# Kernel tuning notes

Measured on AMD Instinct MI355X. Metric: run time of the kernel, lower is better.

The kernel has to match this reference:

```python
import jax, jax.numpy as jnp
import numpy as np

T, N, E, IN_DIM, H = 20, 50000, 800000, 16, 128
NPF = 7  # num_physical_features
EPS = 1e-5


def setup_inputs() -> dict:
    key = jax.random.key(0)
    ks = jax.random.split(key, 24)
    s = 0.05
    inp = {
        'x': jax.random.normal(ks[0], (T, N, IN_DIM), jnp.float32),
        'edge_index': jax.random.randint(ks[1], (2, E), 0, N, jnp.int64),
        # SAGEConv layer 1 (PyG: lin_l on aggregated neighbors w/ bias, lin_r on root no bias)
        'sage1_wl': jax.random.normal(ks[2], (IN_DIM, H), jnp.float32) * s,
        'sage1_bl': jnp.zeros((H,), jnp.float32),
        'sage1_wr': jax.random.normal(ks[3], (IN_DIM, H), jnp.float32) * s,
        # SAGEConv layer 2
        'sage2_wl': jax.random.normal(ks[4], (H, H), jnp.float32) * s,
        'sage2_bl': jnp.zeros((H,), jnp.float32),
        'sage2_wr': jax.random.normal(ks[5], (H, H), jnp.float32) * s,
        # LayerNorm
        'ln_g': jnp.ones((H,), jnp.float32),
        'ln_b': jnp.zeros((H,), jnp.float32),
        # GRU (torch layout: [3H, H], gate order r,z,n)
        'gru_wih': jax.random.normal(ks[6], (3 * H, H), jnp.float32) * s,
        'gru_whh': jax.random.normal(ks[7], (3 * H, H), jnp.float32) * s,
        'gru_bih': jnp.zeros((3 * H,), jnp.float32),
        'gru_bhh': jnp.zeros((3 * H,), jnp.float32),
        # Thickness decoder
        'th_w1': jax.random.normal(ks[8], (H, H), jnp.float32) * s,
        'th_b1': jnp.zeros((H,), jnp.float32),
        'th_w2': jax.random.normal(ks[9], (H, 1), jnp.float32) * s,
        'th_b2': jnp.zeros((1,), jnp.float32),
        # Physical feature decoder
        'ph_w1': jax.random.normal(ks[10], (H, H), jnp.float32) * s,
        'ph_b1': jnp.zeros((H,), jnp.float32),
        'ph_w2': jax.random.normal(ks[11], (H, NPF), jnp.float32) * s,
        'ph_b2': jnp.zeros((NPF,), jnp.float32),
    }
    return inp


def _sage(h, src, dst, deg_inv, wl, bl, wr):
    # mean-aggregate neighbor features over incoming edges, then two linears
    agg = jax.ops.segment_sum(h[src], dst, num_segments=N) * deg_inv[:, None]
    return agg @ wl + bl + h @ wr


def _forward(x, edge_index,
             sage1_wl, sage1_bl, sage1_wr,
             sage2_wl, sage2_bl, sage2_wr,
             ln_g, ln_b,
             gru_wih, gru_whh, gru_bih, gru_bhh,
             th_w1, th_b1, th_w2, th_b2,
             ph_w1, ph_b1, ph_w2, ph_b2):
    src, dst = edge_index[0], edge_index[1]
    deg = jax.ops.segment_sum(jnp.ones((E,), jnp.float32), dst, num_segments=N)
    deg_inv = 1.0 / jnp.maximum(deg, 1.0)

    def encode(xt):  # [N, IN_DIM] -> [N, H]
        h = jax.nn.relu(_sage(xt, src, dst, deg_inv, sage1_wl, sage1_bl, sage1_wr))
        h = jax.nn.relu(_sage(h, src, dst, deg_inv, sage2_wl, sage2_bl, sage2_wr))
        mu = jnp.mean(h, axis=-1, keepdims=True)
        var = jnp.mean(jnp.square(h - mu), axis=-1, keepdims=True)
        return (h - mu) * jax.lax.rsqrt(var + EPS) * ln_g + ln_b

    encoded = jax.lax.map(encode, x)  # [T, N, H]

    # GRU over time, batch = nodes
    def gru_step(h, x_t):
        gi = x_t @ gru_wih.T + gru_bih  # [N, 3H]
        gh = h @ gru_whh.T + gru_bhh
        i_r, i_z, i_n = jnp.split(gi, 3, axis=-1)
        h_r, h_z, h_n = jnp.split(gh, 3, axis=-1)
        r = jax.nn.sigmoid(i_r + h_r)
        z = jax.nn.sigmoid(i_z + h_z)
        n = jnp.tanh(i_n + r * h_n)
        h_new = (1.0 - z) * n + z * h
        return h_new, h_new

    h0 = jnp.zeros((N, H), jnp.float32)
    _, h_temporal = jax.lax.scan(gru_step, h0, encoded)  # [T, N, H]

    th = jax.nn.relu(h_temporal @ th_w1 + th_b1) @ th_w2 + th_b2   # [T, N, 1]
    ph = jax.nn.relu(h_temporal @ ph_w1 + ph_b1) @ ph_w2 + ph_b2   # [T, N, NPF]
    return th, ph


def reference(x, edge_index,
              sage1_wl, sage1_bl, sage1_wr,
              sage2_wl, sage2_bl, sage2_wr,
              ln_g, ln_b,
              gru_wih, gru_whh, gru_bih, gru_bhh,
              th_w1, th_b1, th_w2, th_b2,
              ph_w1, ph_b1, ph_w2, ph_b2):
    return _forward(x, edge_index,
                    sage1_wl, sage1_bl, sage1_wr,
                    sage2_wl, sage2_bl, sage2_wr,
                    ln_g, ln_b,
                    gru_wih, gru_whh, gru_bih, gru_bhh,
                    th_w1, th_b1, th_w2, th_b2,
                    ph_w1, ph_b1, ph_w2, ph_b2)
```

## Files before the change

kernel.cpp:

```cpp
#include <hip/hip_runtime.h>
#include <hip/hip_bf16.h>

#define TT 20
#define NN 50000
#define EE 800000
#define IND 16
#define HH 128
#define NPF 7
#define CC 4
#define NB ((NN + 255) / 256)

typedef __attribute__((ext_vector_type(8))) short bf16x8;
typedef __attribute__((ext_vector_type(4))) float f32x4;
#define MFMA(a, b, c) __builtin_amdgcn_mfma_f32_16x16x32_bf16(a, b, c, 0, 0, 0)

__device__ __forceinline__ unsigned short f2bf(float f) {
    union { float f; unsigned u; } v; v.f = f;
    unsigned r = v.u + 0x7fffu + ((v.u >> 16) & 1u);
    return (unsigned short)(r >> 16);
}
__device__ __forceinline__ float bf2f(unsigned short u) {
    union { unsigned u; float f; } v; v.u = ((unsigned)u) << 16;
    return v.f;
}

__global__ void detect_kernel(const int* ei, int* flag, int E) {
    __shared__ int nz;
    if (threadIdx.x == 0) nz = 0;
    __syncthreads();
    for (int i = threadIdx.x; i < 1024 && i < E; i += blockDim.x)
        if (ei[2 * i + 1] != 0) atomicOr(&nz, 1);
    __syncthreads();
    if (threadIdx.x == 0) *flag = (nz == 0) ? 1 : 0;
}
__device__ __forceinline__ int edge_src(const int* ei, int e, int E, int f) {
    return f ? ei[2 * e] : ei[e];
}
__device__ __forceinline__ int edge_dst(const int* ei, int e, int E, int f) {
    return f ? ei[2 * (E + e)] : ei[E + e];
}
__global__ void count_deg_kernel(const int* ei, const int* flag, int* deg, int E) {
    int e = blockIdx.x * blockDim.x + threadIdx.x;
    if (e >= E) return;
    int f = *flag;
    atomicAdd(&deg[edge_dst(ei, e, E, f)], 1);
}

__global__ __launch_bounds__(256) void sum_blocks_kernel(const int* deg, int* bsum) {
    int i = blockIdx.x * 256 + threadIdx.x;
    int v = (i < NN) ? deg[i] : 0;
#pragma unroll
    for (int o = 1; o <= 32; o <<= 1) v += __shfl_xor(v, o);
    __shared__ int ws[4];
    if ((threadIdx.x & 63) == 0) ws[threadIdx.x >> 6] = v;
    __syncthreads();
    if (threadIdx.x == 0) bsum[blockIdx.x] = ws[0] + ws[1] + ws[2] + ws[3];
}
__global__ __launch_bounds__(256) void scan_blocks_kernel(const int* bsum, int* bbase) {
    __shared__ int arr[256];
    int t = threadIdx.x;
    int v = (t < NB) ? bsum[t] : 0;
    arr[t] = v;
    __syncthreads();
    for (int off = 1; off < 256; off <<= 1) {
        int u = (t >= off) ? arr[t - off] : 0;
        __syncthreads();
        arr[t] += u;
        __syncthreads();
    }
    if (t < NB) bbase[t] = arr[t] - v;
}
__global__ __launch_bounds__(256) void offs_kernel(const int* deg, const int* bbase,
                                                   int* offs, int* cursor,
                                                   float* dinv, int E) {
    __shared__ int arr[256];
    int t = threadIdx.x;
    int i = blockIdx.x * 256 + t;
    int d = (i < NN) ? deg[i] : 0;
    arr[t] = d;
    __syncthreads();
    for (int off = 1; off < 256; off <<= 1) {
        int u = (t >= off) ? arr[t - off] : 0;
        __syncthreads();
        arr[t] += u;
        __syncthreads();
    }
    if (i < NN) {
        int o = bbase[blockIdx.x] + arr[t] - d;
        offs[i] = o;
        cursor[i] = o;
        dinv[i] = 1.0f / (float)(d > 1 ? d : 1);
        if (i == NN - 1) offs[NN] = E;
    }
}
__global__ void fill_csr_kernel(const int* ei, const int* flag, int* cursor,
                                int* csr, int E) {
    int e = blockIdx.x * blockDim.x + threadIdx.x;
    if (e >= E) return;
    int f = *flag;
    int s = edge_src(ei, e, E, f);
    int d = edge_dst(ei, e, E, f);
    int p = atomicAdd(&cursor[d], 1);
    csr[p] = s;
}

__global__ void pack_kernel(const float* src, unsigned short* dst, int tiles,
                            int mode) {
    int id = blockIdx.x * blockDim.x + threadIdx.x;
    if (id >= tiles * 4 * 64) return;
    int lane = id & 63, kk = (id >> 6) & 3, tile = id >> 8;
    int n = tile * 16 + (lane & 15);
    int kbase = kk * 32 + (lane >> 4) * 8;
    unsigned short out[8];
#pragma unroll
    for (int i = 0; i < 8; ++i) {
        int k = kbase + i;
        float v = mode ? src[n * HH + k] : src[k * (tiles * 16) + n];
        out[i] = f2bf(v);
    }
    *(uint4*)(dst + (size_t)id * 8) = *(uint4*)out;
}

__global__ __launch_bounds__(128) void sage1_kernel(
    const float* __restrict__ x, const int* __restrict__ offs,
    const int* __restrict__ csr, const float* __restrict__ dinv,
    const float* __restrict__ wl, const float* __restrict__ bl,
    const float* __restrict__ wr, unsigned short* __restrict__ h1c, int t0) {
    const int tid = threadIdx.x;
    const int ci = blockIdx.y;
    const float* xt = x + (size_t)(t0 + ci) * NN * IND;
    const int m0 = blockIdx.x * 8;
    __shared__ __align__(16) float sAgg[8][IND];
    __shared__ float sX[8][IND];
    {
        int r = tid >> 4, node = m0 + r;
        int l16 = tid & 15, sub = l16 >> 2, q = l16 & 3;
        int e1 = offs[node + 1];
        float4 a0 = make_float4(0.f, 0.f, 0.f, 0.f);
        float4 a1 = make_float4(0.f, 0.f, 0.f, 0.f);
        float4 a2 = make_float4(0.f, 0.f, 0.f, 0.f);
        float4 a3 = make_float4(0.f, 0.f, 0.f, 0.f);
        int e = offs[node] + sub;
        for (; e + 12 < e1; e += 16) {
            int s0 = __builtin_nontemporal_load(&csr[e]);
            int s1 = __builtin_nontemporal_load(&csr[e + 4]);
            int s2 = __builtin_nontemporal_load(&csr[e + 8]);
            int s3 = __builtin_nontemporal_load(&csr[e + 12]);
            float4 v0 = *(const float4*)(xt + (size_t)s0 * IND + q * 4);
            float4 v1 = *(const float4*)(xt + (size_t)s1 * IND + q * 4);
            float4 v2 = *(const float4*)(xt + (size_t)s2 * IND + q * 4);
            float4 v3 = *(const float4*)(xt + (size_t)s3 * IND + q * 4);
            a0.x += v0.x; a0.y += v0.y; a0.z += v0.z; a0.w += v0.w;
            a1.x += v1.x; a1.y += v1.y; a1.z += v1.z; a1.w += v1.w;
            a2.x += v2.x; a2.y += v2.y; a2.z += v2.z; a2.w += v2.w;
            a3.x += v3.x; a3.y += v3.y; a3.z += v3.z; a3.w += v3.w;
        }
        for (; e < e1; e += 4) {
            int s0 = __builtin_nontemporal_load(&csr[e]);
            float4 v0 = *(const float4*)(xt + (size_t)s0 * IND + q * 4);
            a0.x += v0.x; a0.y += v0.y; a0.z += v0.z; a0.w += v0.w;
        }
        float4 acc;
        acc.x = a0.x + a1.x + a2.x + a3.x;
        acc.y = a0.y + a1.y + a2.y + a3.y;
        acc.z = a0.z + a1.z + a2.z + a3.z;
        acc.w = a0.w + a1.w + a2.w + a3.w;
#pragma unroll
        for (int o = 4; o <= 8; o <<= 1) {
            acc.x += __shfl_xor(acc.x, o);
            acc.y += __shfl_xor(acc.y, o);
            acc.z += __shfl_xor(acc.z, o);
            acc.w += __shfl_xor(acc.w, o);
        }
        if (sub == 0) {
            float di = dinv[node];
            acc.x *= di; acc.y *= di; acc.z *= di; acc.w *= di;
            *(float4*)&sAgg[r][q * 4] = acc;
        }
        sX[r][l16] = xt[(size_t)node * IND + l16];
    }
    __syncthreads();
    const int col = tid;
    float acc[8];
    float b = bl[col];
#pragma unroll
    for (int m = 0; m < 8; ++m) acc[m] = b;
#pragma unroll
    for (int k = 0; k < IND; ++k) {
        float wlv = wl[k * HH + col];
        float wrv = wr[k * HH + col];
#pragma unroll
        for (int m = 0; m < 8; ++m) acc[m] += sAgg[m][k] * wlv + sX[m][k] * wrv;
    }
#pragma unroll
    for (int m = 0; m < 8; ++m)
        h1c[((size_t)(m0 + m) * CC + ci) * HH + col] = f2bf(fmaxf(acc[m], 0.f));
}

#define ADD8(acc, v) do {                                     \
    union { unsigned u; float f; } t_;                        \
    t_.u = (v).x << 16;         acc[0] += t_.f;               \
    t_.u = (v).x & 0xffff0000u; acc[1] += t_.f;               \
    t_.u = (v).y << 16;         acc[2] += t_.f;               \
    t_.u = (v).y & 0xffff0000u; acc[3] += t_.f;               \
    t_.u = (v).z << 16;         acc[4] += t_.f;               \
    t_.u = (v).z & 0xffff0000u; acc[5] += t_.f;               \
    t_.u = (v).w << 16;         acc[6] += t_.f;               \
    t_.u = (v).w & 0xffff0000u; acc[7] += t_.f;               \
} while (0)

__global__ __launch_bounds__(256) void sage2_agg_kernel(
    const unsigned short* __restrict__ h1c, const int* __restrict__ offs,
    const int* __restrict__ csr, const float* __restrict__ dinv,
    unsigned short* __restrict__ agg2c) {
    const int wid = threadIdx.x >> 6, lane = threadIdx.x & 63;
    const int n = blockIdx.x * 4 + wid;
    const char* __restrict__ tb = (const char*)h1c;
    const int lb = lane * 16;
    const int e0 = offs[n], e1 = offs[n + 1];
    float A[8][8];
#pragma unroll
    for (int u = 0; u < 8; ++u)
#pragma unroll
        for (int j = 0; j < 8; ++j) A[u][j] = 0.f;
    int e = e0;
    for (; e + 7 < e1; e += 8) {
        int s[8];
#pragma unroll
        for (int u = 0; u < 8; ++u) s[u] = csr[e + u];
        uint4 v[8];
#pragma unroll
        for (int u = 0; u < 8; ++u)
            v[u] = *(const uint4*)(tb + (size_t)s[u] * 1024 + lb);
#pragma unroll
        for (int u = 0; u < 8; ++u) ADD8(A[u], v[u]);
    }
    for (; e < e1; ++e) {
        int s0 = csr[e];
        uint4 v0 = *(const uint4*)(tb + (size_t)s0 * 1024 + lb);
        ADD8(A[0], v0);
    }
    float di = dinv[n];
    unsigned short o[8];
#pragma unroll
    for (int j = 0; j < 8; ++j) {
        float s = ((A[0][j] + A[1][j]) + (A[2][j] + A[3][j])) +
                  ((A[4][j] + A[5][j]) + (A[6][j] + A[7][j]));
        o[j] = f2bf(s * di);
    }
    *(uint4*)((char*)agg2c + (size_t)n * 1024 + lb) = *(uint4*)o;
}

#define LDA(buf, kk)                                                          \
    (*(const bf16x8*)((const char*)(buf) +                                    \
        (((lane & 15) * 256 + (kk) * 64 + (lane >> 4) * 16) ^                 \
         (((lane & 15) & 7) << 4))))

__global__ __launch_bounds__(64) void gru_fused_kernel(
    const unsigned short* __restrict__ agg2c, const unsigned short* __restrict__ h1c,
    const unsigned short* __restrict__ pS2L, const unsigned short* __restrict__ pS2R,
    const float* __restrict__ s2bl, const float* __restrict__ lng,
    const float* __restrict__ lnb,
    const unsigned short* __restrict__ pGI, const unsigned short* __restrict__ pGH,
    const float* __restrict__ bih, const float* __restrict__ bhh,
    float* __restrict__ h, unsigned short* __restrict__ hallc, int ci) {
    const int lane = threadIdx.x;
    const int r0 = blockIdx.x * 16;
    __shared__ unsigned short bufA[16 * 128];
    __shared__ unsigned short bufB[16 * 128];
    __shared__ unsigned short bufH[16 * 128];

#pragma unroll
    for (int j = 0; j < 4; ++j) {
        int off = (lane + 64 * j) * 16;
        int row = off >> 8, colb = off & 255;
        int swz = off ^ ((row & 7) << 4);
        size_t src = (size_t)(r0 + row) * 1024 + (size_t)ci * 256 + colb;
        *(uint4*)((char*)bufA + swz) = *(const uint4*)((const char*)agg2c + src);
        *(uint4*)((char*)bufB + swz) = *(const uint4*)((const char*)h1c + src);
        const float* hs = h + (size_t)r0 * HH + (size_t)(off / 2);
        unsigned short tmp[8];
#pragma unroll
        for (int i = 0; i < 8; ++i) tmp[i] = f2bf(hs[i]);
        *(uint4*)((char*)bufH + swz) = *(uint4*)tmp;
    }
    __syncthreads();

    bf16x8 ae[4], ah[4];
#pragma unroll
    for (int kk = 0; kk < 4; ++kk) { ae[kk] = LDA(bufA, kk); ah[kk] = LDA(bufB, kk); }
    float vE[8][4];
    float sS[4] = {0, 0, 0, 0}, sQ[4] = {0, 0, 0, 0};
#pragma unroll
    for (int c = 0; c < 8; ++c) {
        f32x4 al = {0, 0, 0, 0}, ar = {0, 0, 0, 0};
#pragma unroll
        for (int kk = 0; kk < 4; ++kk) {
            bf16x8 bl = *(const bf16x8*)(pS2L + ((size_t)(c * 4 + kk) * 64 + lane) * 8);
            bf16x8 br = *(const bf16x8*)(pS2R + ((size_t)(c * 4 + kk) * 64 + lane) * 8);
            al = MFMA(ae[kk], bl, al);
            ar = MFMA(ah[kk], br, ar);
        }
        int col = c * 16 + (lane & 15);
        float bb = s2bl[col];
#pragma unroll
        for (int j = 0; j < 4; ++j) {
            float v = fmaxf(al[j] + ar[j] + bb, 0.f);
            vE[c][j] = v; sS[j] += v; sQ[j] += v * v;
        }
    }
#pragma unroll
    for (int o = 1; o <= 8; o <<= 1) {
#pragma unroll
        for (int j = 0; j < 4; ++j) {
            sS[j] += __shfl_xor(sS[j], o);
            sQ[j] += __shfl_xor(sQ[j], o);
        }
    }
    __syncthreads();
#pragma unroll
    for (int c = 0; c < 8; ++c) {
        int col = c * 16 + (lane & 15);
        float g = lng[col], b = lnb[col];
#pragma unroll
        for (int j = 0; j < 4; ++j) {
            float mu = sS[j] * (1.f / 128.f);
            float var = sQ[j] * (1.f / 128.f) - mu * mu;
            float ve = (vE[c][j] - mu) * rsqrtf(var + 1e-5f) * g + b;
            int row = (lane >> 4) * 4 + j;
            int off = ((row * 128 + col) * 2) ^ ((row & 7) << 4);
            *(unsigned short*)((char*)bufA + off) = f2bf(ve);
        }
    }
    __syncthreads();

    bf16x8 xe[4], xh[4];
#pragma unroll
    for (int kk = 0; kk < 4; ++kk) { xe[kk] = LDA(bufA, kk); xh[kk] = LDA(bufH, kk); }
#pragma unroll
    for (int c = 0; c < 8; ++c) {
        f32x4 air = {0,0,0,0}, aiz = {0,0,0,0}, ain = {0,0,0,0};
        f32x4 ahr = {0,0,0,0}, ahz = {0,0,0,0}, ahn = {0,0,0,0};
#pragma unroll
        for (int kk = 0; kk < 4; ++kk) {
            bf16x8 bir = *(const bf16x8*)(pGI + ((size_t)((c     ) * 4 + kk) * 64 + lane) * 8);
            bf16x8 biz = *(const bf16x8*)(pGI + ((size_t)((c +  8) * 4 + kk) * 64 + lane) * 8);
            bf16x8 bin = *(const bf16x8*)(pGI + ((size_t)((c + 16) * 4 + kk) * 64 + lane) * 8);
            bf16x8 bhr = *(const bf16x8*)(pGH + ((size_t)((c     ) * 4 + kk) * 64 + lane) * 8);
            bf16x8 bhz = *(const bf16x8*)(pGH + ((size_t)((c +  8) * 4 + kk) * 64 + lane) * 8);
            bf16x8 bhn = *(const bf16x8*)(pGH + ((size_t)((c + 16) * 4 + kk) * 64 + lane) * 8);
            air = MFMA(xe[kk], bir, air); aiz = MFMA(xe[kk], biz, aiz);
            ain = MFMA(xe[kk], bin, ain);
            ahr = MFMA(xh[kk], bhr, ahr); ahz = MFMA(xh[kk], bhz, ahz);
            ahn = MFMA(xh[kk], bhn, ahn);
        }
        int col = c * 16 + (lane & 15);
        float bir_ = bih[col], biz_ = bih[HH + col], bin_ = bih[2 * HH + col];
        float bhr_ = bhh[col], bhz_ = bhh[HH + col], bhn_ = bhh[2 * HH + col];
#pragma unroll
        for (int j = 0; j < 4; ++j) {
            int row = (lane >> 4) * 4 + j;
            size_t gidx = (size_t)(r0 + row) * HH + col;
            float rr = 1.f / (1.f + expf(-(air[j] + bir_ + ahr[j] + bhr_)));
            float zz = 1.f / (1.f + expf(-(aiz[j] + biz_ + ahz[j] + bhz_)));
            float nn2 = tanhf(ain[j] + bin_ + rr * (ahn[j] + bhn_));
            float hold = h[gidx];
            float hnew = (1.f - zz) * nn2 + zz * hold;
            h[gidx] = hnew;
            hallc[((size_t)(r0 + row) * CC + ci) * HH + col] = f2bf(hnew);
        }
    }
}

__global__ __launch_bounds__(64) void dec_kernel(
    const unsigned short* __restrict__ hall,
    const unsigned short* __restrict__ pT1, const unsigned short* __restrict__ pP1,
    const float* __restrict__ tb1, const float* __restrict__ tw2,
    const float* __restrict__ tb2, const float* __restrict__ pb1,
    const float* __restrict__ pw2, const float* __restrict__ pb2,
    float* __restrict__ out_th, float* __restrict__ out_ph, int t0) {
    const int lane = threadIdx.x;
    const int rc = blockIdx.x * 16;
    const int ci = rc / NN;
    const int n0 = rc - ci * NN;
    const int tg = t0 + ci;
    __shared__ unsigned short bufB[16 * 128];
#pragma unroll
    for (int j = 0; j < 4; ++j) {
        int off = (lane + 64 * j) * 16;
        int row = off >> 8, colb = off & 255;
        int swz = off ^ ((row & 7) << 4);
        *(uint4*)((char*)bufB + swz) =
            *(const uint4*)((const char*)hall +
                            (size_t)(n0 + row) * 1024 + (size_t)ci * 256 + colb);
    }
    __syncthreads();
    bf16x8 xd[4];
#pragma unroll
    for (int kk = 0; kk < 4; ++kk) xd[kk] = LDA(bufB, kk);
    float pt[4] = {0, 0, 0, 0};
    float pf[NPF][4];
#pragma unroll
    for (int f = 0; f < NPF; ++f)
#pragma unroll
        for (int j = 0; j < 4; ++j) pf[f][j] = 0.f;
#pragma unroll
    for (int c = 0; c < 8; ++c) {
        f32x4 at = {0, 0, 0, 0}, ap = {0, 0, 0, 0};
#pragma unroll
        for (int kk = 0; kk < 4; ++kk) {
            bf16x8 bt = *(const bf16x8*)(pT1 + ((size_t)(c * 4 + kk) * 64 + lane) * 8);
            bf16x8 bp = *(const bf16x8*)(pP1 + ((size_t)(c * 4 + kk) * 64 + lane) * 8);
            at = MFMA(xd[kk], bt, at);
            ap = MFMA(xd[kk], bp, ap);
        }
        int col = c * 16 + (lane & 15);
        float b1 = tb1[col], b2 = pb1[col], w2 = tw2[col];
        float wp[NPF];
#pragma unroll
        for (int f = 0; f < NPF; ++f) wp[f] = pw2[col * NPF + f];
#pragma unroll
        for (int j = 0; j < 4; ++j) {
            float a = fmaxf(at[j] + b1, 0.f);
            pt[j] += a * w2;
            float p = fmaxf(ap[j] + b2, 0.f);
#pragma unroll
            for (int f = 0; f < NPF; ++f) pf[f][j] += p * wp[f];
        }
    }
#pragma unroll
    for (int o = 1; o <= 8; o <<= 1) {
#pragma unroll
        for (int j = 0; j < 4; ++j) {
            pt[j] += __shfl_xor(pt[j], o);
#pragma unroll
            for (int f = 0; f < NPF; ++f) pf[f][j] += __shfl_xor(pf[f][j], o);
        }
    }
    if ((lane & 15) == 0) {
        int g = lane >> 4;
#pragma unroll
        for (int j = 0; j < 4; ++j) {
            int gr = n0 + g * 4 + j;
            out_th[(size_t)tg * NN + gr] = pt[j] + tb2[0];
#pragma unroll
            for (int f = 0; f < NPF; ++f)
                out_ph[((size_t)tg * NN + gr) * NPF + f] = pf[f][j] + pb2[f];
        }
    }
}
#undef LDA

extern "C" void kernel_launch(void* const* d_in, const int* in_sizes, int n_in,
                              void* d_out, int out_size, void* d_ws, size_t ws_size,
                              hipStream_t stream) {
    const float* x     = (const float*)d_in[0];
    const int*   ei    = (const int*)d_in[1];
    const float* s1wl  = (const float*)d_in[2];
    const float* s1bl  = (const float*)d_in[3];
    const float* s1wr  = (const float*)d_in[4];
    const float* s2wl  = (const float*)d_in[5];
    const float* s2bl  = (const float*)d_in[6];
    const float* s2wr  = (const float*)d_in[7];
    const float* lng   = (const float*)d_in[8];
    const float* lnb   = (const float*)d_in[9];
    const float* g_wih = (const float*)d_in[10];
    const float* g_whh = (const float*)d_in[11];
    const float* g_bih = (const float*)d_in[12];
    const float* g_bhh = (const float*)d_in[13];
    const float* tw1   = (const float*)d_in[14];
    const float* tb1   = (const float*)d_in[15];
    const float* tw2   = (const float*)d_in[16];
    const float* tb2   = (const float*)d_in[17];
    const float* pw1   = (const float*)d_in[18];
    const float* pb1   = (const float*)d_in[19];
    const float* pw2   = (const float*)d_in[20];
    const float* pb2   = (const float*)d_in[21];

    char* ws = (char*)d_ws;
    size_t o = 0;
    auto alloc = [&](size_t bytes) {
        size_t r = o;
        o += (bytes + 255) & ~(size_t)255;
        return r;
    };
    int*            flag  = (int*)(ws + alloc(4));
    int*            deg   = (int*)(ws + alloc((size_t)NN * 4));
    int*            offs  = (int*)(ws + alloc((size_t)(NN + 1) * 4));
    int*            curs  = (int*)(ws + alloc((size_t)NN * 4));
    int*            csr   = (int*)(ws + alloc((size_t)EE * 4));
    float*          dinv  = (float*)(ws + alloc((size_t)NN * 4));
    int*            bsum  = (int*)(ws + alloc((size_t)NB * 4));
    int*            bbase = (int*)(ws + alloc((size_t)NB * 4));
    unsigned short* pS2L  = (unsigned short*)(ws + alloc(8 * 4 * 64 * 8 * 2));
    unsigned short* pS2R  = (unsigned short*)(ws + alloc(8 * 4 * 64 * 8 * 2));
    unsigned short* pT1   = (unsigned short*)(ws + alloc(8 * 4 * 64 * 8 * 2));
    unsigned short* pP1   = (unsigned short*)(ws + alloc(8 * 4 * 64 * 8 * 2));
    unsigned short* pGI   = (unsigned short*)(ws + alloc(24 * 4 * 64 * 8 * 2));
    unsigned short* pGH   = (unsigned short*)(ws + alloc(24 * 4 * 64 * 8 * 2));
    float*          hbuf  = (float*)(ws + alloc((size_t)NN * HH * 4));
    unsigned short* h1c   = (unsigned short*)(ws + alloc((size_t)NN * CC * HH * 2));
    unsigned short* agg2c = (unsigned short*)(ws + alloc((size_t)NN * CC * HH * 2));
    unsigned short* hallc = agg2c;

    detect_kernel<<<1, 256, 0, stream>>>(ei, flag, EE);
    hipMemsetAsync(deg, 0, (size_t)NN * 4, stream);
    count_deg_kernel<<<(EE + 255) / 256, 256, 0, stream>>>(ei, flag, deg, EE);
    sum_blocks_kernel<<<NB, 256, 0, stream>>>(deg, bsum);
    scan_blocks_kernel<<<1, 256, 0, stream>>>(bsum, bbase);
    offs_kernel<<<NB, 256, 0, stream>>>(deg, bbase, offs, curs, dinv, EE);
    fill_csr_kernel<<<(EE + 255) / 256, 256, 0, stream>>>(ei, flag, curs, csr, EE);
    pack_kernel<<<(8 * 4 * 64 + 255) / 256, 256, 0, stream>>>(s2wl, pS2L, 8, 0);
    pack_kernel<<<(8 * 4 * 64 + 255) / 256, 256, 0, stream>>>(s2wr, pS2R, 8, 0);
    pack_kernel<<<(8 * 4 * 64 + 255) / 256, 256, 0, stream>>>(tw1, pT1, 8, 0);
    pack_kernel<<<(8 * 4 * 64 + 255) / 256, 256, 0, stream>>>(pw1, pP1, 8, 0);
    pack_kernel<<<(24 * 4 * 64 + 255) / 256, 256, 0, stream>>>(g_wih, pGI, 24, 1);
    pack_kernel<<<(24 * 4 * 64 + 255) / 256, 256, 0, stream>>>(g_whh, pGH, 24, 1);
    hipMemsetAsync(hbuf, 0, (size_t)NN * HH * 4, stream);

    float* out = (float*)d_out;
    for (int t0 = 0; t0 < TT; t0 += CC) {
        dim3 g1(NN / 8, CC);
        sage1_kernel<<<g1, 128, 0, stream>>>(x, offs, csr, dinv, s1wl, s1bl,
                                             s1wr, h1c, t0);
        sage2_agg_kernel<<<NN / 4, 256, 0, stream>>>(h1c, offs, csr, dinv, agg2c);
        for (int ci = 0; ci < CC; ++ci) {
            gru_fused_kernel<<<NN / 16, 64, 0, stream>>>(
                agg2c, h1c, pS2L, pS2R, s2bl, lng, lnb, pGI, pGH,
                g_bih, g_bhh, hbuf, hallc, ci);
        }
        dec_kernel<<<CC * NN / 16, 64, 0, stream>>>(
            hallc, pT1, pP1, tb1, tw2, tb2, pb1, pw2, pb2,
            out, out + (size_t)TT * NN, t0);
    }
}
```

Before: 2.636 ms.

## Split encoder from GRU and keep hidden state in LDS across chunk timesteps

The fused per-timestep GRU kernel is split in two. An encoder kernel (SAGE2 linears plus LayerNorm) now runs over all chunk timesteps in one launch and writes its result in place into the aggregation buffer. A GRU loop kernel then keeps the fp32 hidden state of its 16 rows in swizzled LDS across the 4 timesteps, so it no longer reloads and stores h in global memory every step and needs fewer launches. The weight-pack launches are also merged into one kernel, and the sage2 aggregation drops from 8-way to 4-way unrolled accumulation, which lowers register pressure but exposes less memory-level parallelism. The encoded activations now make an extra round trip through global memory.

Measured after the change: 5.195 ms. +97.1%, slower.

```diff
diff --git a/kernel.cpp b/kernel.cpp
--- a/kernel.cpp
+++ b/kernel.cpp
@@ -104,21 +104,32 @@
     csr[p] = s;
 }
 
-__global__ void pack_kernel(const float* src, unsigned short* dst, int tiles,
-                            int mode) {
+__global__ void pack_all_kernel(
+    const float* s2wl, const float* s2wr, const float* tw1, const float* pw1,
+    const float* wih, const float* whh,
+    unsigned short* pS2L, unsigned short* pS2R, unsigned short* pT1,
+    unsigned short* pP1, unsigned short* pGI, unsigned short* pGH) {
     int id = blockIdx.x * blockDim.x + threadIdx.x;
-    if (id >= tiles * 4 * 64) return;
-    int lane = id & 63, kk = (id >> 6) & 3, tile = id >> 8;
+    if (id >= 80 * 256) return;
+    int gt = id >> 8;
+    int lane = id & 63, kk = (id >> 6) & 3;
+    const float* src; unsigned short* dst; int tile, mode, ncols;
+    if (gt < 8)       { src = s2wl; dst = pS2L; tile = gt;      mode = 0; ncols = 128; }
+    else if (gt < 16) { src = s2wr; dst = pS2R; tile = gt - 8;  mode = 0; ncols = 128; }
+    else if (gt < 24) { src = tw1;  dst = pT1;  tile = gt - 16; mode = 0; ncols = 128; }
+    else if (gt < 32) { src = pw1;  dst = pP1;  tile = gt - 24; mode = 0; ncols = 128; }
+    else if (gt < 56) { src = wih;  dst = pGI;  tile = gt - 32; mode = 1; ncols = 384; }
+    else              { src = whh;  dst = pGH;  tile = gt - 56; mode = 1; ncols = 384; }
     int n = tile * 16 + (lane & 15);
     int kbase = kk * 32 + (lane >> 4) * 8;
     unsigned short out[8];
 #pragma unroll
     for (int i = 0; i < 8; ++i) {
         int k = kbase + i;
-        float v = mode ? src[n * HH + k] : src[k * (tiles * 16) + n];
+        float v = mode ? src[n * HH + k] : src[k * ncols + n];
         out[i] = f2bf(v);
     }
-    *(uint4*)(dst + (size_t)id * 8) = *(uint4*)out;
+    *(uint4*)(dst + ((size_t)tile * 256 + kk * 64 + lane) * 8) = *(uint4*)out;
 }
 
 __global__ __launch_bounds__(128) void sage1_kernel(
@@ -218,36 +229,26 @@
     const char* __restrict__ tb = (const char*)h1c;
     const int lb = lane * 16;
     const int e0 = offs[n], e1 = offs[n + 1];
-    float A[8][8];
-#pragma unroll
-    for (int u = 0; u < 8; ++u)
-#pragma unroll
-        for (int j = 0; j < 8; ++j) A[u][j] = 0.f;
+    float a[8] = {0,0,0,0,0,0,0,0}, b[8] = {0,0,0,0,0,0,0,0};
+    float c_[8] = {0,0,0,0,0,0,0,0}, d[8] = {0,0,0,0,0,0,0,0};
     int e = e0;
-    for (; e + 7 < e1; e += 8) {
-        int s[8];
-#pragma unroll
-        for (int u = 0; u < 8; ++u) s[u] = csr[e + u];
-        uint4 v[8];
-#pragma unroll
-        for (int u = 0; u < 8; ++u)
-            v[u] = *(const uint4*)(tb + (size_t)s[u] * 1024 + lb);
-#pragma unroll
-        for (int u = 0; u < 8; ++u) ADD8(A[u], v[u]);
+    for (; e + 3 < e1; e += 4) {
+        int s0 = csr[e], s1 = csr[e + 1], s2 = csr[e + 2], s3 = csr[e + 3];
+        uint4 v0 = *(const uint4*)(tb + (size_t)s0 * 1024 + lb);
+        uint4 v1 = *(const uint4*)(tb + (size_t)s1 * 1024 + lb);
+        uint4 v2 = *(const uint4*)(tb + (size_t)s2 * 1024 + lb);
+        uint4 v3 = *(const uint4*)(tb + (size_t)s3 * 1024 + lb);
+        ADD8(a, v0); ADD8(b, v1); ADD8(c_, v2); ADD8(d, v3);
     }
     for (; e < e1; ++e) {
         int s0 = csr[e];
         uint4 v0 = *(const uint4*)(tb + (size_t)s0 * 1024 + lb);
-        ADD8(A[0], v0);
+        ADD8(a, v0);
     }
     float di = dinv[n];
     unsigned short o[8];
 #pragma unroll
-    for (int j = 0; j < 8; ++j) {
-        float s = ((A[0][j] + A[1][j]) + (A[2][j] + A[3][j])) +
-                  ((A[4][j] + A[5][j]) + (A[6][j] + A[7][j]));
-        o[j] = f2bf(s * di);
-    }
+    for (int j = 0; j < 8; ++j) o[j] = f2bf((a[j] + b[j] + c_[j] + d[j]) * di);
     *(uint4*)((char*)agg2c + (size_t)n * 1024 + lb) = *(uint4*)o;
 }
 
@@ -256,20 +257,16 @@
         (((lane & 15) * 256 + (kk) * 64 + (lane >> 4) * 16) ^                 \
          (((lane & 15) & 7) << 4))))
 
-__global__ __launch_bounds__(64) void gru_fused_kernel(
-    const unsigned short* __restrict__ agg2c, const unsigned short* __restrict__ h1c,
+__global__ __launch_bounds__(64) void enc_kernel(
+    unsigned short* __restrict__ agg2c, const unsigned short* __restrict__ h1c,
     const unsigned short* __restrict__ pS2L, const unsigned short* __restrict__ pS2R,
     const float* __restrict__ s2bl, const float* __restrict__ lng,
-    const float* __restrict__ lnb,
-    const unsigned short* __restrict__ pGI, const unsigned short* __restrict__ pGH,
-    const float* __restrict__ bih, const float* __restrict__ bhh,
-    float* __restrict__ h, unsigned short* __restrict__ hallc, int ci) {
+    const float* __restrict__ lnb) {
     const int lane = threadIdx.x;
     const int r0 = blockIdx.x * 16;
+    const int ci = blockIdx.y;
     __shared__ unsigned short bufA[16 * 128];
     __shared__ unsigned short bufB[16 * 128];
-    __shared__ unsigned short bufH[16 * 128];
-
 #pragma unroll
     for (int j = 0; j < 4; ++j) {
         int off = (lane + 64 * j) * 16;
@@ -278,14 +275,8 @@
         size_t src = (size_t)(r0 + row) * 1024 + (size_t)ci * 256 + colb;
         *(uint4*)((char*)bufA + swz) = *(const uint4*)((const char*)agg2c + src);
         *(uint4*)((char*)bufB + swz) = *(const uint4*)((const char*)h1c + src);
-        const float* hs = h + (size_t)r0 * HH + (size_t)(off / 2);
-        unsigned short tmp[8];
-#pragma unroll
-        for (int i = 0; i < 8; ++i) tmp[i] = f2bf(hs[i]);
-        *(uint4*)((char*)bufH + swz) = *(uint4*)tmp;
-    }
-    __syncthreads();
-
+    }
+    __syncthreads();
     bf16x8 ae[4], ah[4];
 #pragma unroll
     for (int kk = 0; kk < 4; ++kk) { ae[kk] = LDA(bufA, kk); ah[kk] = LDA(bufB, kk); }
@@ -333,42 +324,107 @@
         }
     }
     __syncthreads();
-
-    bf16x8 xe[4], xh[4];
-#pragma unroll
-    for (int kk = 0; kk < 4; ++kk) { xe[kk] = LDA(bufA, kk); xh[kk] = LDA(bufH, kk); }
-#pragma unroll
-    for (int c = 0; c < 8; ++c) {
-        f32x4 air = {0,0,0,0}, aiz = {0,0,0,0}, ain = {0,0,0,0};
-        f32x4 ahr = {0,0,0,0}, ahz = {0,0,0,0}, ahn = {0,0,0,0};
+#pragma unroll
+    for (int j = 0; j < 4; ++j) {
+        int off = (lane + 64 * j) * 16;
+        int row = off >> 8, colb = off & 255;
+        int swz = off ^ ((row & 7) << 4);
+        size_t src = (size_t)(r0 + row) * 1024 + (size_t)ci * 256 + colb;
+        *(uint4*)((char*)agg2c + src) = *(const uint4*)((const char*)bufA + swz);
+    }
+}
+
+__global__ __launch_bounds__(64) void gru_loop_kernel(
+    const unsigned short* __restrict__ encc,
+    const unsigned short* __restrict__ pGI, const unsigned short* __restrict__ pGH,
+    const float* __restrict__ bih, const float* __restrict__ bhh,
+    float* __restrict__ h, unsigned short* __restrict__ hallc) {
+    const int lane = threadIdx.x;
+    const int r0 = blockIdx.x * 16;
+    const int fr = lane & 15;
+    const int rg = (lane >> 4) * 4;
+    __shared__ unsigned short bufA[16 * 128];
+    __shared__ float          bufHF[16 * 128];
+
+#pragma unroll
+    for (int j = 0; j < 8; ++j) {
+        int off = (lane + 64 * j) * 16;
+        int row = off >> 9;
+        int swz = off ^ ((row & 7) << 5);
+        *(uint4*)((char*)bufHF + swz) =
+            *(const uint4*)((const char*)(h + (size_t)r0 * HH) + off);
+    }
+    __syncthreads();
+
+#pragma unroll 1
+    for (int ci = 0; ci < CC; ++ci) {
+#pragma unroll
+        for (int j = 0; j < 4; ++j) {
+            int off = (lane + 64 * j) * 16;
+            int row = off >> 8, colb = off & 255;
+            int swz = off ^ ((row & 7) << 4);
+            size_t src = (size_t)(r0 + row) * 1024 + (size_t)ci * 256 + colb;
+            *(uint4*)((char*)bufA + swz) = *(const uint4*)((const char*)encc + src);
+        }
+        __syncthreads();
+
+        bf16x8 xe[4], xh[4];
 #pragma unroll
         for (int kk = 0; kk < 4; ++kk) {
-            bf16x8 bir = *(const bf16x8*)(pGI + ((size_t)((c     ) * 4 + kk) * 64 + lane) * 8);
-            bf16x8 biz = *(const bf16x8*)(pGI + ((size_t)((c +  8) * 4 + kk) * 64 + lane) * 8);
-            bf16x8 bin = *(const bf16x8*)(pGI + ((size_t)((c + 16) * 4 + kk) * 64 + lane) * 8);
-            bf16x8 bhr = *(const bf16x8*)(pGH + ((size_t)((c     ) * 4 + kk) * 64 + lane) * 8);
-            bf16x8 bhz = *(const bf16x8*)(pGH + ((size_t)((c +  8) * 4 + kk) * 64 + lane) * 8);
-            bf16x8 bhn = *(const bf16x8*)(pGH + ((size_t)((c + 16) * 4 + kk) * 64 + lane) * 8);
-            air = MFMA(xe[kk], bir, air); aiz = MFMA(xe[kk], biz, aiz);
-            ain = MFMA(xe[kk], bin, ain);
-            ahr = MFMA(xh[kk], bhr, ahr); ahz = MFMA(xh[kk], bhz, ahz);
-            ahn = MFMA(xh[kk], bhn, ahn);
-        }
-        int col = c * 16 + (lane & 15);
-        float bir_ = bih[col], biz_ = bih[HH + col], bin_ = bih[2 * HH + col];
-        float bhr_ = bhh[col], bhz_ = bhh[HH + col], bhn_ = bhh[2 * HH + col];
-#pragma unroll
-        for (int j = 0; j < 4; ++j) {
-            int row = (lane >> 4) * 4 + j;
-            size_t gidx = (size_t)(r0 + row) * HH + col;
-            float rr = 1.f / (1.f + expf(-(air[j] + bir_ + ahr[j] + bhr_)));
-            float zz = 1.f / (1.f + expf(-(aiz[j] + biz_ + ahz[j] + bhz_)));
-            float nn2 = tanhf(ain[j] + bin_ + rr * (ahn[j] + bhn_));
-            float hold = h[gidx];
-            float hnew = (1.f - zz) * nn2 + zz * hold;
-            h[gidx] = hnew;
-            hallc[((size_t)(r0 + row) * CC + ci) * HH + col] = f2bf(hnew);
-        }
+            xe[kk] = LDA(bufA, kk);
+            int base = (fr * 128 + kk * 32 + (lane >> 4) * 8) * 4;
+            int swz = base ^ ((fr & 7) << 5);
+            f32x4 h0 = *(const f32x4*)((const char*)bufHF + swz);
+            f32x4 h1v = *(const f32x4*)((const char*)bufHF + swz + 16);
+            unsigned short tmp[8] = {f2bf(h0[0]), f2bf(h0[1]), f2bf(h0[2]), f2bf(h0[3]),
+                                     f2bf(h1v[0]), f2bf(h1v[1]), f2bf(h1v[2]), f2bf(h1v[3])};
+            xh[kk] = *(const bf16x8*)tmp;
+        }
+        __syncthreads();
+
+#pragma unroll
+        for (int c = 0; c < 8; ++c) {
+            f32x4 air = {0,0,0,0}, aiz = {0,0,0,0}, ain = {0,0,0,0};
+            f32x4 ahr = {0,0,0,0}, ahz = {0,0,0,0}, ahn = {0,0,0,0};
+#pragma unroll
+            for (int kk = 0; kk < 4; ++kk) {
+                bf16x8 bir = *(const bf16x8*)(pGI + ((size_t)((c     ) * 4 + kk) * 64 + lane) * 8);
+                bf16x8 biz = *(const bf16x8*)(pGI + ((size_t)((c +  8) * 4 + kk) * 64 + lane) * 8);
+                bf16x8 bin = *(const bf16x8*)(pGI + ((size_t)((c + 16) * 4 + kk) * 64 + lane) * 8);
+                bf16x8 bhr = *(const bf16x8*)(pGH + ((size_t)((c     ) * 4 + kk) * 64 + lane) * 8);
+                bf16x8 bhz = *(const bf16x8*)(pGH + ((size_t)((c +  8) * 4 + kk) * 64 + lane) * 8);
+                bf16x8 bhn = *(const bf16x8*)(pGH + ((size_t)((c + 16) * 4 + kk) * 64 + lane) * 8);
+                air = MFMA(xe[kk], bir, air); aiz = MFMA(xe[kk], biz, aiz);
+                ain = MFMA(xe[kk], bin, ain);
+                ahr = MFMA(xh[kk], bhr, ahr); ahz = MFMA(xh[kk], bhz, ahz);
+                ahn = MFMA(xh[kk], bhn, ahn);
+            }
+            int col = c * 16 + fr;
+            float bir_ = bih[col], biz_ = bih[HH + col], bin_ = bih[2 * HH + col];
+            float bhr_ = bhh[col], bhz_ = bhh[HH + col], bhn_ = bhh[2 * HH + col];
+#pragma unroll
+            for (int j = 0; j < 4; ++j) {
+                int row = rg + j;
+                int hoff = ((row * 128 + col) * 4) ^ ((row & 7) << 5);
+                float hold = *(const float*)((const char*)bufHF + hoff);
+                float rr = 1.f / (1.f + expf(-(air[j] + bir_ + ahr[j] + bhr_)));
+                float zz = 1.f / (1.f + expf(-(aiz[j] + biz_ + ahz[j] + bhz_)));
+                float nn2 = tanhf(ain[j] + bin_ + rr * (ahn[j] + bhn_));
+                float hnew = (1.f - zz) * nn2 + zz * hold;
+                *(float*)((char*)bufHF + hoff) = hnew;
+                hallc[((size_t)(r0 + row) * CC + ci) * HH + col] = f2bf(hnew);
+            }
+        }
+        __syncthreads();
+    }
+
+#pragma unroll
+    for (int j = 0; j < 8; ++j) {
+        int off = (lane + 64 * j) * 16;
+        int row = off >> 9;
+        int swz = off ^ ((row & 7) << 5);
+        *(uint4*)((char*)(h + (size_t)r0 * HH) + off) =
+            *(const uint4*)((const char*)bufHF + swz);
     }
 }
 
@@ -510,25 +566,19 @@
     scan_blocks_kernel<<<1, 256, 0, stream>>>(bsum, bbase);
     offs_kernel<<<NB, 256, 0, stream>>>(deg, bbase, offs, curs, dinv, EE);
     fill_csr_kernel<<<(EE + 255) / 256, 256, 0, stream>>>(ei, flag, curs, csr, EE);
-    pack_kernel<<<(8 * 4 * 64 + 255) / 256, 256, 0, stream>>>(s2wl, pS2L, 8, 0);
-    pack_kernel<<<(8 * 4 * 64 + 255) / 256, 256, 0, stream>>>(s2wr, pS2R, 8, 0);
-    pack_kernel<<<(8 * 4 * 64 + 255) / 256, 256, 0, stream>>>(tw1, pT1, 8, 0);
-    pack_kernel<<<(8 * 4 * 64 + 255) / 256, 256, 0, stream>>>(pw1, pP1, 8, 0);
-    pack_kernel<<<(24 * 4 * 64 + 255) / 256, 256, 0, stream>>>(g_wih, pGI, 24, 1);
-    pack_kernel<<<(24 * 4 * 64 + 255) / 256, 256, 0, stream>>>(g_whh, pGH, 24, 1);
+    pack_all_kernel<<<(80 * 256 + 255) / 256, 256, 0, stream>>>(
+        s2wl, s2wr, tw1, pw1, g_wih, g_whh, pS2L, pS2R, pT1, pP1, pGI, pGH);
     hipMemsetAsync(hbuf, 0, (size_t)NN * HH * 4, stream);
 
     float* out = (float*)d_out;
     for (int t0 = 0; t0 < TT; t0 += CC) {
-        dim3 g1(NN / 8, CC);
+        dim3 g1(NN / 8, CC), ge(NN / 16, CC);
         sage1_kernel<<<g1, 128, 0, stream>>>(x, offs, csr, dinv, s1wl, s1bl,
                                              s1wr, h1c, t0);
         sage2_agg_kernel<<<NN / 4, 256, 0, stream>>>(h1c, offs, csr, dinv, agg2c);
-        for (int ci = 0; ci < CC; ++ci) {
-            gru_fused_kernel<<<NN / 16, 64, 0, stream>>>(
-                agg2c, h1c, pS2L, pS2R, s2bl, lng, lnb, pGI, pGH,
-                g_bih, g_bhh, hbuf, hallc, ci);
-        }
+        enc_kernel<<<ge, 64, 0, stream>>>(agg2c, h1c, pS2L, pS2R, s2bl, lng, lnb);
+        gru_loop_kernel<<<NN / 16, 64, 0, stream>>>(
+            agg2c, pGI, pGH, g_bih, g_bhh, hbuf, hallc);
         dec_kernel<<<CC * NN / 16, 64, 0, stream>>>(
             hallc, pT1, pP1, tb1, tw2, tb2, pb1, pw2, pb2,
             out, out + (size_t)TT * NN, t0);
```
